# Performance work log

Hardware: AMD Instinct MI355X
Metric: run time of the kernel (lower is better)

Reference implementation:

```python
import jax, jax.numpy as jnp
import numpy as np

N = 20000      # nodes
E = 320000     # edges (avg degree 16)
IN = 128
HID = 64
CLS = 32
H0, H1, H2 = 4, 4, 6
SLOPE = 0.2


def _lin(key, fan_in, fan_out):
    kw, kb = jax.random.split(key)
    s = 1.0 / np.sqrt(fan_in)
    W = jax.random.uniform(kw, (fan_in, fan_out), minval=-s, maxval=s, dtype=jnp.float32)
    b = jax.random.uniform(kb, (fan_out,), minval=-s, maxval=s, dtype=jnp.float32)
    return W, b


def setup_inputs() -> dict:
    key = jax.random.key(0)
    ks = jax.random.split(key, 16)
    x = jax.random.normal(ks[0], (N, IN), dtype=jnp.float32)
    src = jax.random.randint(ks[1], (E,), 0, N)
    dst = jax.random.randint(ks[2], (E,), 0, N)
    W0s, b0s = _lin(ks[3], IN, H0 * HID)
    W0d, b0d = _lin(ks[4], IN, H0 * HID)
    a0 = jax.random.normal(ks[5], (H0, HID), dtype=jnp.float32) * 0.05
    d1 = H0 * HID  # 256, flattened hidden width
    W1s, b1s = _lin(ks[6], d1, H1 * HID)
    W1d, b1d = _lin(ks[7], d1, H1 * HID)
    a1 = jax.random.normal(ks[8], (H1, HID), dtype=jnp.float32) * 0.05
    W2s, b2s = _lin(ks[9], d1, H2 * CLS)
    W2d, b2d = _lin(ks[10], d1, H2 * CLS)
    a2 = jax.random.normal(ks[11], (H2, CLS), dtype=jnp.float32) * 0.05
    Wr2, br2 = _lin(ks[12], d1, H2 * CLS)  # residual projection (256 != 192)
    return dict(x=x, src=src, dst=dst,
                W0s=W0s, b0s=b0s, W0d=W0d, b0d=b0d, a0=a0,
                W1s=W1s, b1s=b1s, W1d=W1d, b1d=b1d, a1=a1,
                W2s=W2s, b2s=b2s, W2d=W2d, b2d=b2d, a2=a2,
                Wr2=Wr2, br2=br2)


def _gatv2_layer(x, src, dst, Ws, bs, Wd, bd, attn, heads, dim, res, act):
    n = x.shape[0]
    feat_src = (x @ Ws + bs).reshape(n, heads, dim)
    feat_dst = (x @ Wd + bd).reshape(n, heads, dim)
    # GATv2 edge scores: a^T LeakyReLU(W_l h_u + W_r h_v)
    e = jax.nn.leaky_relu(feat_src[src] + feat_dst[dst], SLOPE)  # [E,H,D]
    logits = jnp.einsum('ehd,hd->eh', e, attn)                    # [E,H]
    # numerically-stable edge softmax over incoming edges per destination
    m = jax.ops.segment_max(logits, dst, num_segments=n)
    m = jnp.where(jnp.isfinite(m), m, 0.0)
    ex = jnp.exp(logits - m[dst])
    denom = jax.ops.segment_sum(ex, dst, num_segments=n)
    alpha = ex / denom[dst]                                        # [E,H]
    out = jax.ops.segment_sum(feat_src[src] * alpha[:, :, None], dst, num_segments=n)
    if res == 'id':
        out = out + x.reshape(n, heads, dim)
    elif res is not None:
        Wr, br = res
        out = out + (x @ Wr + br).reshape(n, heads, dim)
    if act:
        out = jax.nn.elu(out)
    return out  # [n, heads, dim]


def reference(x, src, dst,
              W0s, b0s, W0d, b0d, a0,
              W1s, b1s, W1d, b1d, a1,
              W2s, b2s, W2d, b2d, a2,
              Wr2, br2):
    h = _gatv2_layer(x, src, dst, W0s, b0s, W0d, b0d, a0, H0, HID, None, True)
    h = h.reshape(N, H0 * HID)
    h = _gatv2_layer(h, src, dst, W1s, b1s, W1d, b1d, a1, H1, HID, 'id', True)
    h = h.reshape(N, H1 * HID)
    out = _gatv2_layer(h, src, dst, W2s, b2s, W2d, b2d, a2, H2, CLS, (Wr2, br2), False)
    return out.mean(axis=1)  # [N, num_classes]
```

## Files before the change

kernel.cpp:

```cpp
#include <hip/hip_runtime.h>
#include <hip/hip_bf16.h>
#include <float.h>
#include <math.h>

#define NN 20000
#define EE 320000
#define IN_DIM 128
#define SLOPE_ 0.2f
#define DEG_CAP 64

typedef __attribute__((ext_vector_type(4))) float f32x4;
typedef _Float16 f16;
typedef __attribute__((ext_vector_type(2))) _Float16 f16x2;
typedef __attribute__((ext_vector_type(4))) _Float16 f16x4;
typedef __attribute__((ext_vector_type(8))) _Float16 f16x8;
typedef unsigned short ushort;

__device__ inline void prep_elem(const float* __restrict__ Wa, const float* __restrict__ ba, int na,
                                 const float* __restrict__ Wb, const float* __restrict__ bb, int nb,
                                 const float* __restrict__ Wc, const float* __restrict__ bc, int nc,
                                 int K, f16* __restrict__ Wt, float* __restrict__ bias_cat, int idx) {
    int n = idx / K;
    int k = idx - n * K;
    const float* W; const float* b; int nl; int ncols;
    if (n < na) { W = Wa; b = ba; nl = n; ncols = na; }
    else if (n < na + nb) { W = Wb; b = bb; nl = n - na; ncols = nb; }
    else { W = Wc; b = bc; nl = n - na - nb; ncols = nc; }
    Wt[(size_t)n * K + k] = (f16)W[(size_t)k * ncols + nl];
    if (k == 0) bias_cat[n] = b[nl];
}

#define SEG0 (512 * 128)
#define SEG1 (512 * 256)
#define SEG2 (576 * 256)
#define SEG3 (NN * IN_DIM / 4)
#define SEG4 (EE)
__global__ void prep_all(const float* __restrict__ W0s, const float* __restrict__ b0s,
                         const float* __restrict__ W0d, const float* __restrict__ b0d,
                         const float* __restrict__ W1s, const float* __restrict__ b1s,
                         const float* __restrict__ W1d, const float* __restrict__ b1d,
                         const float* __restrict__ W2s, const float* __restrict__ b2s,
                         const float* __restrict__ W2d, const float* __restrict__ b2d,
                         const float* __restrict__ Wr2, const float* __restrict__ br2,
                         const float* __restrict__ x,
                         const int* __restrict__ src, const int* __restrict__ dst,
                         f16* __restrict__ Wt0, float* __restrict__ bias0,
                         f16* __restrict__ Wt1, float* __restrict__ bias1,
                         f16* __restrict__ Wt2, float* __restrict__ bias2,
                         f16* __restrict__ A, unsigned int* __restrict__ deg,
                         int* __restrict__ csr_src) {
    int idx = blockIdx.x * 256 + threadIdx.x;
    if (idx < SEG0) {
        prep_elem(W0s, b0s, 256, W0d, b0d, 256, nullptr, nullptr, 0, 128, Wt0, bias0, idx);
    } else if ((idx -= SEG0) < SEG1) {
        prep_elem(W1s, b1s, 256, W1d, b1d, 256, nullptr, nullptr, 0, 256, Wt1, bias1, idx);
    } else if ((idx -= SEG1) < SEG2) {
        prep_elem(W2s, b2s, 192, W2d, b2d, 192, Wr2, br2, 192, 256, Wt2, bias2, idx);
    } else if ((idx -= SEG2) < SEG3) {
        float4 v = ((const float4*)x)[idx];
        f16x4 o = {(f16)v.x, (f16)v.y, (f16)v.z, (f16)v.w};
        ((f16x4*)A)[idx] = o;
    } else if ((idx -= SEG3) < SEG4) {
        int d = dst[idx];
        unsigned int pos = atomicAdd(&deg[d], 1u);
        csr_src[(unsigned)d * DEG_CAP + pos] = src[idx];
    }
}

__global__ __launch_bounds__(256) void gemm_mfma_f16(
        const f16* __restrict__ A, const f16* __restrict__ Wt,
        const float* __restrict__ bias,
        f16* __restrict__ F0, f16* __restrict__ F1, float* __restrict__ F2,
        int b1, int b2, int M, int K, int S, int gx, int gy) {
    __shared__ f16 Bs[64 * 256];
    __shared__ f16 Cs[4][32 * 66];

    const int bid = blockIdx.x;
    const int p = bid & 7;
    const int q = bid >> 3;
    const int bn_i = q % gx;
    const int bm_i = (q / gx) * 8 + p;
    if (bm_i >= gy) return;
    const int bm = bm_i * 256;
    const int bn = bn_i * 64;

    const int tid = threadIdx.x;
    const int wave = tid >> 6;
    const int lane = tid & 63;
    const int m16 = lane & 15;
    const int quad = lane >> 4;

    {
        const int n = tid >> 2;
        const int q0 = tid & 3;
        for (int j = 0; j * 32 < K; ++j) {
            int k0 = j * 32 + q0 * 8;
            f16x8 v = *(const f16x8*)(Wt + (size_t)(bn + n) * K + k0);
            int chunk = (j * 4 + (n >> 4)) * 64 + q0 * 16 + (n & 15);
            *(f16x8*)&Bs[chunk * 8] = v;
        }
    }
    __syncthreads();

    const int rb0 = bm + wave * 64;
    f32x4 acc[2][2][4];
    #pragma unroll
    for (int mi = 0; mi < 2; ++mi)
        #pragma unroll
        for (int mt = 0; mt < 2; ++mt)
            #pragma unroll
            for (int nt = 0; nt < 4; ++nt) acc[mi][mt][nt] = (f32x4){0.f, 0.f, 0.f, 0.f};

    int ar[2][2];
    #pragma unroll
    for (int mi = 0; mi < 2; ++mi)
        #pragma unroll
        for (int mt = 0; mt < 2; ++mt) {
            int row = rb0 + mi * 32 + mt * 16 + m16;
            ar[mi][mt] = row < M ? row : M - 1;
        }

    #pragma unroll 2
    for (int k0 = 0; k0 < K; k0 += 32) {
        f16x8 bs[4];
        #pragma unroll
        for (int nt = 0; nt < 4; ++nt)
            bs[nt] = *(const f16x8*)&Bs[(((k0 >> 5) * 4 + nt) * 64 + lane) * 8];
        #pragma unroll
        for (int mi = 0; mi < 2; ++mi) {
            f16x8 ah[2];
            #pragma unroll
            for (int mt = 0; mt < 2; ++mt)
                ah[mt] = *(const f16x8*)(A + (size_t)ar[mi][mt] * K + k0 + quad * 8);
            #pragma unroll
            for (int nt = 0; nt < 4; ++nt)
                #pragma unroll
                for (int mt = 0; mt < 2; ++mt)
                    acc[mi][mt][nt] = __builtin_amdgcn_mfma_f32_16x16x32_f16(ah[mt], bs[nt], acc[mi][mt][nt], 0, 0, 0);
        }
    }

    #pragma unroll
    for (int mi = 0; mi < 2; ++mi) {
        const int rbase = rb0 + mi * 32;
        if (bn < b2) {
            f16* __restrict__ Fb;
            int cs, cb;
            if (bn >= b1) { Fb = F1; cb = bn - b1; cs = b2 - b1; }
            else          { Fb = F0; cb = bn;      cs = b1; }
            f16* cw = &Cs[wave][0];
            #pragma unroll
            for (int nt = 0; nt < 4; ++nt) {
                float bv = bias[bn + nt * 16 + m16];
                #pragma unroll
                for (int mt = 0; mt < 2; ++mt)
                    #pragma unroll
                    for (int r = 0; r < 4; ++r) {
                        int row = mt * 16 + quad * 4 + r;
                        cw[row * 66 + nt * 16 + m16] = (f16)(acc[mi][mt][nt][r] + bv);
                    }
            }
            int lrow = lane >> 1;
            int lcol = (lane & 1) * 32;
            int grow = rbase + lrow;
            if (grow < M) {
                #pragma unroll
                for (int j = 0; j < 4; ++j) {
                    f16x8 v = *(f16x8*)&cw[lrow * 66 + lcol + j * 8];
                    *(f16x8*)&Fb[(size_t)grow * cs + cb + lcol + j * 8] = v;
                }
            }
        } else {
            int cs = S - b2;
            #pragma unroll
            for (int nt = 0; nt < 4; ++nt) {
                int col = bn - b2 + nt * 16 + m16;
                float bv = bias[bn + nt * 16 + m16];
                #pragma unroll
                for (int mt = 0; mt < 2; ++mt)
                    #pragma unroll
                    for (int r = 0; r < 4; ++r) {
                        int row = rbase + mt * 16 + quad * 4 + r;
                        if (row < M) F2[(size_t)row * cs + col] = acc[mi][mt][nt][r] + bv;
                    }
            }
        }
    }
}

#define AGG_STEP4(U0)                                                         \
    _Pragma("unroll")                                                         \
    for (int uu = 0; uu < 4; ++uu) {                                          \
        const int u = (U0) + uu;                                              \
        const f16x8 cur = buf[u];                                             \
        buf[u] = *(const f16x8*)&fsb[(unsigned)cidx[u] * HD + off];           \
        cidx[u] = csr_src[min(jj0 + b + 16 + u, last)];                       \
        float p = 0.f;                                                        \
        _Pragma("unroll")                                                     \
        for (int i = 0; i < 4; ++i) {                                         \
            f16x2 cp = (f16x2){cur[2 * i], cur[2 * i + 1]};                   \
            f16x2 xp = cp + fdp[i];                                           \
            unsigned xu = __builtin_bit_cast(unsigned, xp) & 0x7FFF7FFFu;     \
            f16x2 xa = __builtin_bit_cast(f16x2, xu);                         \
            p = __builtin_amdgcn_fdot2(xp, a6p[i], p, false);                 \
            p = __builtin_amdgcn_fdot2(xa, a4p[i], p, false);                 \
        }                                                                     \
        _Pragma("unroll")                                                     \
        for (int o = 1; o < GSZ; o <<= 1) p += __shfl_xor(p, o, 64);          \
        float w = (b + u < deg) ? __expf(p) : 0.f;                            \
        lh += w;                                                              \
        _Pragma("unroll")                                                     \
        for (int d = 0; d < 8; ++d) acc[d] += w * (float)cur[d];              \
    }

template <int HD, int D, bool HAS_RES, bool DO_ELU, int OUT_MODE>
__global__ __launch_bounds__(256) void gat_node_aggregate(
        const f16* __restrict__ fsb, const f16* __restrict__ fdb,
        const float* __restrict__ attn,
        const unsigned int* __restrict__ degv,
        const int* __restrict__ csr_src,
        const float* __restrict__ resid, int RS,
        float* __restrict__ outF, f16* __restrict__ outA) {
    constexpr int LANES = HD / 8;
    constexpr int GSZ = D / 8;
    __shared__ float red[(OUT_MODE == 2) ? 8 : 1][(OUT_MODE == 2) ? HD : 1];

    const int wave = threadIdx.x >> 6;
    const int lane = threadIdx.x & 63;
    const int half = lane >> 5;
    const int ln = lane & 31;
    const int t = blockIdx.x * 8 + wave * 2 + half;
    const bool active = (ln < LANES);
    const unsigned off = active ? 8u * ln : 0u;

    f16x2 fdp[4], a6p[4], a4p[4];
    if (active) {
        f16x8 dv = *(const f16x8*)&fdb[(unsigned)t * HD + off];
        float4 aA = *(const float4*)&attn[off];
        float4 aB = *(const float4*)&attn[off + 4];
        float av[8] = {aA.x, aA.y, aA.z, aA.w, aB.x, aB.y, aB.z, aB.w};
        #pragma unroll
        for (int i = 0; i < 4; ++i) {
            fdp[i] = (f16x2){dv[2 * i], dv[2 * i + 1]};
            a6p[i] = (f16x2){(f16)(0.6f * av[2 * i]), (f16)(0.6f * av[2 * i + 1])};
            a4p[i] = (f16x2){(f16)(0.4f * av[2 * i]), (f16)(0.4f * av[2 * i + 1])};
        }
    } else {
        #pragma unroll
        for (int i = 0; i < 4; ++i) {
            fdp[i] = (f16x2){0, 0};
            a6p[i] = (f16x2){0, 0};
            a4p[i] = (f16x2){0, 0};
        }
    }

    const int jj0 = t * DEG_CAP;
    const int deg = (int)degv[t];
    const int last = jj0 + deg - 1;
    const int degO = __shfl_xor(deg, 32, 64);
    const int mdeg = max(deg, degO);

    float acc[8];
    #pragma unroll
    for (int d = 0; d < 8; ++d) acc[d] = 0.f;
    float lh = 0.f;

    f16x8 buf[8];
    int cidx[8];
    #pragma unroll
    for (int u = 0; u < 8; ++u) {
        int e0 = max(min(jj0 + u, last), 0);
        buf[u] = *(const f16x8*)&fsb[(unsigned)csr_src[e0] * HD + off];
        cidx[u] = csr_src[max(min(jj0 + 8 + u, last), 0)];
    }

    for (int b = 0; b < mdeg; b += 8) {
        AGG_STEP4(0)
        if (b + 4 < mdeg) {
            AGG_STEP4(4)
        }
    }

    float inv = (lh > 0.f) ? 1.f / lh : 0.f;
    float vout[8];
    #pragma unroll
    for (int d = 0; d < 8; ++d) vout[d] = acc[d] * inv;
    if (HAS_RES && active) {
        float4 rA = *(const float4*)&resid[(unsigned)t * RS + off];
        float4 rB = *(const float4*)&resid[(unsigned)t * RS + off + 4];
        vout[0] += rA.x; vout[1] += rA.y; vout[2] += rA.z; vout[3] += rA.w;
        vout[4] += rB.x; vout[5] += rB.y; vout[6] += rB.z; vout[7] += rB.w;
    }
    if (DO_ELU) {
        #pragma unroll
        for (int d = 0; d < 8; ++d) vout[d] = vout[d] > 0.f ? vout[d] : expm1f(vout[d]);
    }

    if (OUT_MODE == 2) {
        const int nib = wave * 2 + half;
        if (active) {
            *(float4*)&red[nib][off] = make_float4(vout[0], vout[1], vout[2], vout[3]);
            *(float4*)&red[nib][off + 4] = make_float4(vout[4], vout[5], vout[6], vout[7]);
        }
        __syncthreads();
        int node = threadIdx.x >> 5;
        int col = threadIdx.x & 31;
        float ssum = 0.f;
        #pragma unroll
        for (int h = 0; h < 6; ++h) ssum += red[node][h * 32 + col];
        outF[(unsigned)(blockIdx.x * 8 + node) * 32 + col] = ssum * (1.f / 6.f);
    } else if (active) {
        f16x8 av;
        #pragma unroll
        for (int d = 0; d < 8; ++d) av[d] = (f16)vout[d];
        *(f16x8*)&outA[(unsigned)t * HD + off] = av;
        if (OUT_MODE == 0) {
            *(float4*)&outF[(unsigned)t * HD + off] = make_float4(vout[0], vout[1], vout[2], vout[3]);
            *(float4*)&outF[(unsigned)t * HD + off + 4] = make_float4(vout[4], vout[5], vout[6], vout[7]);
        }
    }
}

extern "C" void kernel_launch(void* const* d_in, const int* in_sizes, int n_in,
                              void* d_out, int out_size, void* d_ws, size_t ws_size,
                              hipStream_t stream) {
    const float* x   = (const float*)d_in[0];
    const int*   src = (const int*)d_in[1];
    const int*   dst = (const int*)d_in[2];
    const float* W0s = (const float*)d_in[3];
    const float* b0s = (const float*)d_in[4];
    const float* W0d = (const float*)d_in[5];
    const float* b0d = (const float*)d_in[6];
    const float* a0  = (const float*)d_in[7];
    const float* W1s = (const float*)d_in[8];
    const float* b1s = (const float*)d_in[9];
    const float* W1d = (const float*)d_in[10];
    const float* b1d = (const float*)d_in[11];
    const float* a1  = (const float*)d_in[12];
    const float* W2s = (const float*)d_in[13];
    const float* b2s = (const float*)d_in[14];
    const float* W2d = (const float*)d_in[15];
    const float* b2d = (const float*)d_in[16];
    const float* a2  = (const float*)d_in[17];
    const float* Wr2 = (const float*)d_in[18];
    const float* br2 = (const float*)d_in[19];

    f16* FsH = (f16*)d_ws;
    f16* FdH = FsH + (size_t)NN * 256;
    f16* A   = FdH + (size_t)NN * 256;
    float* O0 = (float*)(A + (size_t)NN * 256);
    f16* Wt0 = (f16*)(O0 + (size_t)NN * 256);
    f16* Wt1 = Wt0 + 512 * 128;
    f16* Wt2 = Wt1 + 512 * 256;
    float* bias0 = (float*)(Wt2 + 576 * 256);
    float* bias1 = bias0 + 512;
    float* bias2 = bias1 + 512;
    unsigned int* deg = (unsigned int*)(bias2 + 576);
    int* csr_src      = (int*)(deg + NN);

    hipMemsetAsync(deg, 0, (size_t)NN * 4 + (size_t)NN * DEG_CAP * 4, stream);

    {
        int total = SEG0 + SEG1 + SEG2 + SEG3 + SEG4;
        prep_all<<<(total + 255) / 256, 256, 0, stream>>>(
            W0s, b0s, W0d, b0d, W1s, b1s, W1d, b1d, W2s, b2s, W2d, b2d, Wr2, br2, x,
            src, dst, Wt0, bias0, Wt1, bias1, Wt2, bias2, A, deg, csr_src);
    }

    const int gy = (NN + 255) / 256;
    const int gy8 = ((gy + 7) / 8) * 8;
    const int nagg = NN / 8;

    gemm_mfma_f16<<<gy8 * 8, 256, 0, stream>>>(A, Wt0, bias0,
                                               FsH, FdH, nullptr, 256, 512, NN, 128, 512, 8, gy);
    gat_node_aggregate<256, 64, false, true, 0><<<nagg, 256, 0, stream>>>(
        FsH, FdH, a0, deg, csr_src, nullptr, 0, O0, A);

    gemm_mfma_f16<<<gy8 * 8, 256, 0, stream>>>(A, Wt1, bias1,
                                               FsH, FdH, nullptr, 256, 512, NN, 256, 512, 8, gy);
    gat_node_aggregate<256, 64, true, true, 1><<<nagg, 256, 0, stream>>>(
        FsH, FdH, a1, deg, csr_src, O0, 256, nullptr, A);

    gemm_mfma_f16<<<gy8 * 9, 256, 0, stream>>>(A, Wt2, bias2,
                                               FsH, FdH, O0, 192, 384, NN, 256, 576, 9, gy);
    gat_node_aggregate<192, 32, true, false, 2><<<nagg, 256, 0, stream>>>(
        FsH, FdH, a2, deg, csr_src, O0, 192, (float*)d_out, nullptr);
}
```

Baseline: 285.3 us.

## Shrink GEMM row tile, reuse B smem for epilogue, skip CSR memset

The GEMM block now covers 128 rows instead of 256, with each wave doing 32 rows, which doubles the grid. The epilogue staging buffer now reuses the B shared-memory tile after a barrier, lowering LDS per block and possibly raising occupancy. The memset of the padded CSR array is dropped; degree is clamped to DEG_CAP and out-of-range source indices are guarded so stale entries are never used. The trade-off is that each block reloads the full B tile for half as many rows, and edges beyond DEG_CAP per node are silently dropped.

```diff
diff --git a/kernel.cpp b/kernel.cpp
--- a/kernel.cpp
+++ b/kernel.cpp
@@ -6,7 +6,6 @@
 #define NN 20000
 #define EE 320000
 #define IN_DIM 128
-#define SLOPE_ 0.2f
 #define DEG_CAP 64
 
 typedef __attribute__((ext_vector_type(4))) float f32x4;
@@ -14,12 +13,11 @@
 typedef __attribute__((ext_vector_type(2))) _Float16 f16x2;
 typedef __attribute__((ext_vector_type(4))) _Float16 f16x4;
 typedef __attribute__((ext_vector_type(8))) _Float16 f16x8;
-typedef unsigned short ushort;
-
-__device__ inline void prep_elem(const float* __restrict__ Wa, const float* __restrict__ ba, int na,
-                                 const float* __restrict__ Wb, const float* __restrict__ bb, int nb,
-                                 const float* __restrict__ Wc, const float* __restrict__ bc, int nc,
-                                 int K, f16* __restrict__ Wt, float* __restrict__ bias_cat, int idx) {
+
+__device__ __forceinline__ void prep_elem(const float* __restrict__ Wa, const float* __restrict__ ba, int na,
+                                          const float* __restrict__ Wb, const float* __restrict__ bb, int nb,
+                                          const float* __restrict__ Wc, const float* __restrict__ bc, int nc,
+                                          int K, f16* __restrict__ Wt, float* __restrict__ bias_cat, int idx) {
     int n = idx / K;
     int k = idx - n * K;
     const float* W; const float* b; int nl; int ncols;
@@ -63,7 +61,7 @@
     } else if ((idx -= SEG3) < SEG4) {
         int d = dst[idx];
         unsigned int pos = atomicAdd(&deg[d], 1u);
-        csr_src[(unsigned)d * DEG_CAP + pos] = src[idx];
+        if (pos < DEG_CAP) csr_src[(unsigned)d * DEG_CAP + pos] = src[idx];
     }
 }
 
@@ -73,7 +71,6 @@
         f16* __restrict__ F0, f16* __restrict__ F1, float* __restrict__ F2,
         int b1, int b2, int M, int K, int S, int gx, int gy) {
     __shared__ f16 Bs[64 * 256];
-    __shared__ f16 Cs[4][32 * 66];
 
     const int bid = blockIdx.x;
     const int p = bid & 7;
@@ -81,7 +78,7 @@
     const int bn_i = q % gx;
     const int bm_i = (q / gx) * 8 + p;
     if (bm_i >= gy) return;
-    const int bm = bm_i * 256;
+    const int bm = bm_i * 128;
     const int bn = bn_i * 64;
 
     const int tid = threadIdx.x;
@@ -102,88 +99,80 @@
     }
     __syncthreads();
 
-    const int rb0 = bm + wave * 64;
-    f32x4 acc[2][2][4];
-    #pragma unroll
-    for (int mi = 0; mi < 2; ++mi)
-        #pragma unroll
-        for (int mt = 0; mt < 2; ++mt)
-            #pragma unroll
-            for (int nt = 0; nt < 4; ++nt) acc[mi][mt][nt] = (f32x4){0.f, 0.f, 0.f, 0.f};
-
-    int ar[2][2];
-    #pragma unroll
-    for (int mi = 0; mi < 2; ++mi)
-        #pragma unroll
-        for (int mt = 0; mt < 2; ++mt) {
-            int row = rb0 + mi * 32 + mt * 16 + m16;
-            ar[mi][mt] = row < M ? row : M - 1;
-        }
-
-    #pragma unroll 2
+    const int rb0 = bm + wave * 32;
+    f32x4 acc[2][4];
+    #pragma unroll
+    for (int mt = 0; mt < 2; ++mt)
+        #pragma unroll
+        for (int nt = 0; nt < 4; ++nt) acc[mt][nt] = (f32x4){0.f, 0.f, 0.f, 0.f};
+
+    int ar[2];
+    #pragma unroll
+    for (int mt = 0; mt < 2; ++mt) {
+        int row = rb0 + mt * 16 + m16;
+        ar[mt] = row < M ? row : M - 1;
+    }
+
+    #pragma unroll 4
     for (int k0 = 0; k0 < K; k0 += 32) {
         f16x8 bs[4];
         #pragma unroll
         for (int nt = 0; nt < 4; ++nt)
             bs[nt] = *(const f16x8*)&Bs[(((k0 >> 5) * 4 + nt) * 64 + lane) * 8];
-        #pragma unroll
-        for (int mi = 0; mi < 2; ++mi) {
-            f16x8 ah[2];
+        f16x8 ah[2];
+        #pragma unroll
+        for (int mt = 0; mt < 2; ++mt)
+            ah[mt] = *(const f16x8*)(A + (size_t)ar[mt] * K + k0 + quad * 8);
+        #pragma unroll
+        for (int nt = 0; nt < 4; ++nt)
             #pragma unroll
             for (int mt = 0; mt < 2; ++mt)
-                ah[mt] = *(const f16x8*)(A + (size_t)ar[mi][mt] * K + k0 + quad * 8);
+                acc[mt][nt] = __builtin_amdgcn_mfma_f32_16x16x32_f16(ah[mt], bs[nt], acc[mt][nt], 0, 0, 0);
+    }
+
+    __syncthreads();
+    f16* Cs = Bs;
+
+    if (bn < b2) {
+        f16* __restrict__ Fb;
+        int cs, cb;
+        if (bn >= b1) { Fb = F1; cb = bn - b1; cs = b2 - b1; }
+        else          { Fb = F0; cb = bn;      cs = b1; }
+        f16* cw = Cs + wave * (32 * 66);
+        #pragma unroll
+        for (int nt = 0; nt < 4; ++nt) {
+            float bv = bias[bn + nt * 16 + m16];
             #pragma unroll
-            for (int nt = 0; nt < 4; ++nt)
+            for (int mt = 0; mt < 2; ++mt)
                 #pragma unroll
-                for (int mt = 0; mt < 2; ++mt)
-                    acc[mi][mt][nt] = __builtin_amdgcn_mfma_f32_16x16x32_f16(ah[mt], bs[nt], acc[mi][mt][nt], 0, 0, 0);
-        }
-    }
-
-    #pragma unroll
-    for (int mi = 0; mi < 2; ++mi) {
-        const int rbase = rb0 + mi * 32;
-        if (bn < b2) {
-            f16* __restrict__ Fb;
-            int cs, cb;
-            if (bn >= b1) { Fb = F1; cb = bn - b1; cs = b2 - b1; }
-            else          { Fb = F0; cb = bn;      cs = b1; }
-            f16* cw = &Cs[wave][0];
+                for (int r = 0; r < 4; ++r) {
+                    int row = mt * 16 + quad * 4 + r;
+                    cw[row * 66 + nt * 16 + m16] = (f16)(acc[mt][nt][r] + bv);
+                }
+        }
+        int lrow = lane >> 1;
+        int lcol = (lane & 1) * 32;
+        int grow = rb0 + lrow;
+        if (grow < M) {
             #pragma unroll
-            for (int nt = 0; nt < 4; ++nt) {
-                float bv = bias[bn + nt * 16 + m16];
+            for (int j = 0; j < 4; ++j) {
+                f16x8 v = *(f16x8*)&cw[lrow * 66 + lcol + j * 8];
+                *(f16x8*)&Fb[(size_t)grow * cs + cb + lcol + j * 8] = v;
+            }
+        }
+    } else {
+        int cs = S - b2;
+        #pragma unroll
+        for (int nt = 0; nt < 4; ++nt) {
+            int col = bn - b2 + nt * 16 + m16;
+            float bv = bias[bn + nt * 16 + m16];
+            #pragma unroll
+            for (int mt = 0; mt < 2; ++mt)
                 #pragma unroll
-                for (int mt = 0; mt < 2; ++mt)
-                    #pragma unroll
-                    for (int r = 0; r < 4; ++r) {
-                        int row = mt * 16 + quad * 4 + r;
-                        cw[row * 66 + nt * 16 + m16] = (f16)(acc[mi][mt][nt][r] + bv);
-                    }
-            }
-            int lrow = lane >> 1;
-            int lcol = (lane & 1) * 32;
-            int grow = rbase + lrow;
-            if (grow < M) {
-                #pragma unroll
-                for (int j = 0; j < 4; ++j) {
-                    f16x8 v = *(f16x8*)&cw[lrow * 66 + lcol + j * 8];
-                    *(f16x8*)&Fb[(size_t)grow * cs + cb + lcol + j * 8] = v;
+                for (int r = 0; r < 4; ++r) {
+                    int row = rb0 + mt * 16 + quad * 4 + r;
+                    if (row < M) F2[(size_t)row * cs + col] = acc[mt][nt][r] + bv;
                 }
-            }
-        } else {
-            int cs = S - b2;
-            #pragma unroll
-            for (int nt = 0; nt < 4; ++nt) {
-                int col = bn - b2 + nt * 16 + m16;
-                float bv = bias[bn + nt * 16 + m16];
-                #pragma unroll
-                for (int mt = 0; mt < 2; ++mt)
-                    #pragma unroll
-                    for (int r = 0; r < 4; ++r) {
-                        int row = rbase + mt * 16 + quad * 4 + r;
-                        if (row < M) F2[(size_t)row * cs + col] = acc[mi][mt][nt][r] + bv;
-                    }
-            }
         }
     }
 }
@@ -193,21 +182,22 @@
     for (int uu = 0; uu < 4; ++uu) {                                          \
         const int u = (U0) + uu;                                              \
         const f16x8 cur = buf[u];                                             \
-        buf[u] = *(const f16x8*)&fsb[(unsigned)cidx[u] * HD + off];           \
-        cidx[u] = csr_src[min(jj0 + b + 16 + u, last)];                       \
-        float p = 0.f;                                                        \
+        unsigned su = (unsigned)cidx[u]; su = su < NN ? su : 0u;              \
+        buf[u] = *(const f16x8*)&fsb[su * (unsigned)HD + off];                \
+        cidx[u] = csr_src[max(min(jj0 + b + 16 + u, last), 0)];               \
+        float pp = 0.f;                                                       \
         _Pragma("unroll")                                                     \
         for (int i = 0; i < 4; ++i) {                                         \
             f16x2 cp = (f16x2){cur[2 * i], cur[2 * i + 1]};                   \
             f16x2 xp = cp + fdp[i];                                           \
             unsigned xu = __builtin_bit_cast(unsigned, xp) & 0x7FFF7FFFu;     \
             f16x2 xa = __builtin_bit_cast(f16x2, xu);                         \
-            p = __builtin_amdgcn_fdot2(xp, a6p[i], p, false);                 \
-            p = __builtin_amdgcn_fdot2(xa, a4p[i], p, false);                 \
+            pp = __builtin_amdgcn_fdot2(xp, a6p[i], pp, false);               \
+            pp = __builtin_amdgcn_fdot2(xa, a4p[i], pp, false);               \
         }                                                                     \
         _Pragma("unroll")                                                     \
-        for (int o = 1; o < GSZ; o <<= 1) p += __shfl_xor(p, o, 64);          \
-        float w = (b + u < deg) ? __expf(p) : 0.f;                            \
+        for (int o = 1; o < GSZ; o <<= 1) pp += __shfl_xor(pp, o, 64);        \
+        float w = (b + u < dg) ? __expf(pp) : 0.f;                            \
         lh += w;                                                              \
         _Pragma("unroll")                                                     \
         for (int d = 0; d < 8; ++d) acc[d] += w * (float)cur[d];              \
@@ -248,17 +238,15 @@
     } else {
         #pragma unroll
         for (int i = 0; i < 4; ++i) {
-            fdp[i] = (f16x2){0, 0};
-            a6p[i] = (f16x2){0, 0};
-            a4p[i] = (f16x2){0, 0};
+            fdp[i] = (f16x2){0, 0}; a6p[i] = (f16x2){0, 0}; a4p[i] = (f16x2){0, 0};
         }
     }
 
     const int jj0 = t * DEG_CAP;
-    const int deg = (int)degv[t];
-    const int last = jj0 + deg - 1;
-    const int degO = __shfl_xor(deg, 32, 64);
-    const int mdeg = max(deg, degO);
+    const int dg = min((int)degv[t], DEG_CAP);
+    const int last = jj0 + dg - 1;
+    const int degO = __shfl_xor(dg, 32, 64);
+    const int mdeg = max(dg, degO);
 
     float acc[8];
     #pragma unroll
@@ -270,7 +258,8 @@
     #pragma unroll
     for (int u = 0; u < 8; ++u) {
         int e0 = max(min(jj0 + u, last), 0);
-        buf[u] = *(const f16x8*)&fsb[(unsigned)csr_src[e0] * HD + off];
+        unsigned s0 = (unsigned)csr_src[e0]; s0 = s0 < NN ? s0 : 0u;
+        buf[u] = *(const f16x8*)&fsb[s0 * (unsigned)HD + off];
         cidx[u] = csr_src[max(min(jj0 + 8 + u, last), 0)];
     }
 
@@ -358,8 +347,7 @@
     unsigned int* deg = (unsigned int*)(bias2 + 576);
     int* csr_src      = (int*)(deg + NN);
 
-    hipMemsetAsync(deg, 0, (size_t)NN * 4 + (size_t)NN * DEG_CAP * 4, stream);
-
+    hipMemsetAsync(deg, 0, (size_t)NN * 4, stream);
     {
         int total = SEG0 + SEG1 + SEG2 + SEG3 + SEG4;
         prep_all<<<(total + 255) / 256, 256, 0, stream>>>(
@@ -367,7 +355,7 @@
             src, dst, Wt0, bias0, Wt1, bias1, Wt2, bias2, A, deg, csr_src);
     }
 
-    const int gy = (NN + 255) / 256;
+    const int gy = (NN + 127) / 128;
     const int gy8 = ((gy + 7) / 8) * 8;
     const int nagg = NN / 8;
 
```

Result: slower. 295.8 us (+3.7%).
